# Kernel tuning notes

Hardware: AMD Instinct MI355X
Metric: run time of the kernel (lower is better)

Reference implementation:

```python
import jax, jax.numpy as jnp
import numpy as np

N_USER = 100000
M_ITEM = 50000
N_NODE = N_USER + M_ITEM
D = 64           # latent_dim
WD = D // 2      # word_emb_dim
FU = FI = 10     # padded feature-bag width
NUF = NIF = 30000
VOCAB = 20000
T = 8            # tokens per text source (name/comment/comment_list)
DNU = DNI = 10   # numeric feature dims
B = 2048         # seed batch
S = 20           # sampled neighbors per layer
L = 2            # num_layers


def setup_inputs() -> dict:
    key = jax.random.key(0)
    ks = jax.random.split(key, 26)
    f = lambda i, s: jax.random.normal(ks[i], s, jnp.float32) * 0.05
    ri = lambda i, s, hi: jax.random.randint(ks[i], s, 0, hi)
    return {
        # int (graph / lookup) inputs
        "seeds": ri(0, (B,), N_USER),
        "neigh1": ri(1, (B, S), N_NODE),
        "neigh2": ri(2, (B, S, S), N_NODE),
        "user_feat_idx": ri(3, (N_USER, FU), NUF),
        "item_feat_idx": ri(4, (M_ITEM, FI), NIF),
        "user_text_idx": ri(5, (N_USER, 3, T), VOCAB),
        "item_text_idx": ri(6, (M_ITEM, 3, T), VOCAB),
        # float tables / features
        "user_id_emb": f(7, (N_USER, D)),
        "item_id_emb": f(8, (M_ITEM, D)),
        "user_feat_emb": f(9, (NUF, D)),
        "item_feat_emb": f(10, (NIF, D)),
        "word_emb": f(11, (VOCAB, WD)),
        "user_word300": f(12, (N_USER, 300)),
        "item_word300": f(13, (M_ITEM, 300)),
        "item_sent768": f(14, (M_ITEM, 768)),
        "user_numeric": f(15, (N_USER, DNU)),
        "item_numeric": f(16, (M_ITEM, DNI)),
        # linears (stored as (in, out); y = x @ W + b)
        "Wnum_u": f(17, (DNU, D)), "bnum_u": jnp.zeros((D,), jnp.float32),
        "Wnum_i": f(18, (DNI, D)), "bnum_i": jnp.zeros((D,), jnp.float32),
        "Wproj_u": f(19, (int(D * 3.5) + 300, D)), "bproj_u": jnp.zeros((D,), jnp.float32),
        "Wproj_i": f(20, (int(D * 3.5) + 300 + 768, D)), "bproj_i": jnp.zeros((D,), jnp.float32),
        "W_w": f(21, (L, 2 * D, D)), "b_w": jnp.zeros((L, D), jnp.float32),
        "W_v": f(22, (L, D, D)), "b_v": jnp.zeros((L, D), jnp.float32),
    }


def _forward(user_id_emb, item_id_emb, user_feat_emb, item_feat_emb, word_emb,
             user_word300, item_word300, item_sent768, user_numeric, item_numeric,
             Wnum_u, bnum_u, Wnum_i, bnum_i, Wproj_u, bproj_u, Wproj_i, bproj_i,
             W_w, b_w, W_v, b_v,
             seeds, neigh1, neigh2, user_feat_idx, item_feat_idx,
             user_text_idx, item_text_idx):
    # --- multi-source node embeddings (get_text_embedding + proj + numeric) ---
    # text: mean-pool word embeddings per source, concat 3 sources -> 1.5*D
    u_text = word_emb[user_text_idx].mean(axis=2).reshape(N_USER, 3 * WD)
    i_text = word_emb[item_text_idx].mean(axis=2).reshape(M_ITEM, 3 * WD)
    # feature bags: mean-pooled embedding lookup
    u_feat = user_feat_emb[user_feat_idx].mean(axis=1)
    i_feat = item_feat_emb[item_feat_idx].mean(axis=1)
    u = (jnp.concatenate([user_id_emb, u_feat, u_text, user_word300], -1) @ Wproj_u
         + bproj_u + user_numeric @ Wnum_u + bnum_u)
    it = (jnp.concatenate([item_id_emb, i_feat, i_text, item_word300, item_sent768], -1) @ Wproj_i
          + bproj_i + item_numeric @ Wnum_i + bnum_i)
    x = jnp.concatenate([u, it], axis=0)  # [N_NODE, D], items offset by N_USER

    # --- neighbor-sampled GraphSAGE: h = W_l([self, mean(V_l(neigh))]) ---
    def sage(l, self_x, neigh_x, act):
        agg = (neigh_x @ W_v[l] + b_v[l]).mean(axis=-2)
        h = jnp.concatenate([self_x, agg], axis=-1) @ W_w[l] + b_w[l]
        return jax.nn.relu(h) if act else h

    x0 = x[seeds]        # [B, D]
    x1 = x[neigh1]       # [B, S, D]
    x2 = x[neigh2]       # [B, S, S, D]
    h1 = sage(0, x1, x2, True)   # layer-0 applied to 1-hop nodes
    h0 = sage(0, x0, x1, True)   # layer-0 applied to seeds
    out = sage(1, h0, h1, False)  # final layer, no activation
    return out  # [B, D]


def reference(seeds, neigh1, neigh2, user_feat_idx, item_feat_idx, user_text_idx,
              item_text_idx, user_id_emb, item_id_emb, user_feat_emb, item_feat_emb,
              word_emb, user_word300, item_word300, item_sent768, user_numeric,
              item_numeric, Wnum_u, bnum_u, Wnum_i, bnum_i, Wproj_u, bproj_u,
              Wproj_i, bproj_i, W_w, b_w, W_v, b_v):
    return _forward(user_id_emb, item_id_emb, user_feat_emb, item_feat_emb, word_emb,
                    user_word300, item_word300, item_sent768, user_numeric, item_numeric,
                    Wnum_u, bnum_u, Wnum_i, bnum_i, Wproj_u, bproj_u, Wproj_i, bproj_i,
                    W_w, b_w, W_v, b_v,
                    seeds, neigh1, neigh2, user_feat_idx, item_feat_idx,
                    user_text_idx, item_text_idx)
```

## Files before the change

kernel.cpp:

```cpp
#include <hip/hip_runtime.h>
#include <stdint.h>

#define N_USER 100000
#define M_ITEM 50000
#define N_NODE 150000
#define B_SEED 2048
#define S_NB 20
#define UBLK 6250
#define IBLK 3125

typedef __bf16   bf16x8 __attribute__((ext_vector_type(8)));
typedef float    f32x4  __attribute__((ext_vector_type(4)));
typedef uint32_t u32x4  __attribute__((ext_vector_type(4)));

__device__ __forceinline__ uint16_t f2bf(float f) {
    uint32_t u = __float_as_uint(f);
    return (uint16_t)((u + 0x7FFFu + ((u >> 16) & 1u)) >> 16);
}
__device__ __forceinline__ uint32_t pack2bf(float a, float b) {
    return (uint32_t)f2bf(a) | ((uint32_t)f2bf(b) << 16);
}
__device__ __forceinline__ float bf2f(uint16_t u) {
    return __uint_as_float(((uint32_t)u) << 16);
}

union BF8 { bf16x8 v; uint32_t u[4]; };

__device__ __forceinline__ bf16x8 pack8(const float4 lo, const float4 hi) {
    BF8 r;
    r.u[0] = pack2bf(lo.x, lo.y); r.u[1] = pack2bf(lo.z, lo.w);
    r.u[2] = pack2bf(hi.x, hi.y); r.u[3] = pack2bf(hi.z, hi.w);
    return r.v;
}
__device__ __forceinline__ bf16x8 ldf32x8_mask(const float* rowp, int base, int limit) {
    BF8 r;
#pragma unroll
    for (int h = 0; h < 4; ++h) {
        const int k0 = base + 2 * h;
        const float a = (k0     < limit) ? rowp[k0]     : 0.f;
        const float b = (k0 + 1 < limit) ? rowp[k0 + 1] : 0.f;
        r.u[h] = pack2bf(a, b);
    }
    return r.v;
}

__global__ void prep_kernel(const float* __restrict__ Wproj_u, const float* __restrict__ Wnum_u,
                            const float* __restrict__ Wproj_i, const float* __restrict__ Wnum_i,
                            const float* __restrict__ Wv0, const float* __restrict__ Ww0,
                            uint16_t* __restrict__ WTU, uint16_t* __restrict__ WTI,
                            uint16_t* __restrict__ WvT, uint16_t* __restrict__ WwT)
{
    const int idx = blockIdx.x * 256 + threadIdx.x;
    if (idx < 36864) {
        const int d = idx / 576, kp = idx - d * 576;
        float v = 0.f;
        if (kp < 160)      v = Wproj_u[(64 + kp) * 64 + d];
        else if (kp < 224) v = Wproj_u[(kp - 160) * 64 + d];
        else if (kp < 256) { const int j = kp - 224; if (j < 10)  v = Wnum_u[j * 64 + d]; }
        else               { const int j = kp - 256; if (j < 300) v = Wproj_u[(224 + j) * 64 + d]; }
        WTU[d * 576 + kp] = f2bf(v);
    } else if (idx < 122880) {
        const int i2 = idx - 36864;
        const int d = i2 / 1344, kp = i2 - d * 1344;
        float v = 0.f;
        if (kp < 160)      v = Wproj_i[(64 + kp) * 64 + d];
        else if (kp < 224) v = Wproj_i[(kp - 160) * 64 + d];
        else if (kp < 256) { const int j = kp - 224; if (j < 10)  v = Wnum_i[j * 64 + d]; }
        else if (kp < 576) { const int j = kp - 256; if (j < 300) v = Wproj_i[(224 + j) * 64 + d]; }
        else               { const int j = kp - 576; v = Wproj_i[(524 + j) * 64 + d]; }
        WTI[d * 1344 + kp] = f2bf(v);
    } else {
        const int i2 = idx - 122880;
        if (i2 < 4096) { const int d = i2 >> 6, k = i2 & 63;  WvT[d * 64 + k]  = f2bf(Wv0[k * 64 + d]); }
        else           { const int j = i2 - 4096;
                         const int d = j >> 7, k = j & 127;   WwT[d * 128 + k] = f2bf(Ww0[k * 64 + d]); }
    }
}

__global__ __launch_bounds__(256, 4) void proj_kernel(
    const float* __restrict__ u_id,  const int* __restrict__ ufi,
    const float* __restrict__ ufe,   const int* __restrict__ uti,
    const float* __restrict__ i_id,  const int* __restrict__ ifi,
    const float* __restrict__ ife,   const int* __restrict__ iti,
    const float* __restrict__ word_emb,
    const float* __restrict__ uw300, const float* __restrict__ iw300,
    const float* __restrict__ is768,
    const float* __restrict__ unum,  const float* __restrict__ inum,
    const uint16_t* __restrict__ WTU, const uint16_t* __restrict__ WTI,
    const float* __restrict__ bproj_u, const float* __restrict__ bnum_u,
    const float* __restrict__ bproj_i, const float* __restrict__ bnum_i,
    uint16_t* __restrict__ xout)
{
    __shared__ float R[4 * 16 * 64];

    const int t = threadIdx.x;
    const int w = t >> 6, l = t & 63;
    const int l15 = l & 15, g4 = l >> 4;
    const bool item = blockIdx.x >= UBLK;
    const int tile = item ? (blockIdx.x - UBLK) : blockIdx.x;
    const int nloc = tile * 16 + l15;

    const float* id_emb   = item ? i_id  : u_id;
    const int*   feat_idx = item ? ifi   : ufi;
    const float* feat_emb = item ? ife   : ufe;
    const int*   text_idx = item ? iti   : uti;
    const float* word300  = item ? iw300 : uw300;
    const float* numeric  = item ? inum  : unum;
    const uint16_t* WT    = item ? WTI   : WTU;
    const int KPADP       = item ? 1344  : 576;

    f32x4 acc[4] = {};
    const uint16_t* WTp[4];
#pragma unroll
    for (int db = 0; db < 4; ++db)
        WTp[db] = WT + (size_t)(db * 16 + l15) * KPADP + g4 * 8;

    auto MM = [&](bf16x8 af, int kb) {
#pragma unroll
        for (int db = 0; db < 4; ++db) {
            const bf16x8 bfr = *reinterpret_cast<const bf16x8*>(WTp[db] + kb);
            acc[db] = __builtin_amdgcn_mfma_f32_16x16x32_bf16(af, bfr, acc[db], 0, 0, 0);
        }
    };

    if (w < 2) {
        const int* fip = feat_idx + (size_t)nloc * 10;
        int fi[10];
#pragma unroll
        for (int j = 0; j < 10; ++j) fi[j] = fip[j];
        float4 s0 = make_float4(0.f, 0.f, 0.f, 0.f);
        float4 s1 = make_float4(0.f, 0.f, 0.f, 0.f);
#pragma unroll
        for (int j = 0; j < 10; ++j) {
            const float* rp = feat_emb + (size_t)fi[j] * 64 + w * 32 + g4 * 8;
            const float4 a = *(const float4*)rp;
            const float4 b = *(const float4*)(rp + 4);
            s0.x += a.x; s0.y += a.y; s0.z += a.z; s0.w += a.w;
            s1.x += b.x; s1.y += b.y; s1.z += b.z; s1.w += b.w;
        }
        MM(pack8(make_float4(s0.x * 0.1f, s0.y * 0.1f, s0.z * 0.1f, s0.w * 0.1f),
                 make_float4(s1.x * 0.1f, s1.y * 0.1f, s1.z * 0.1f, s1.w * 0.1f)),
           w * 32);
    }

    {
        const int src = (w == 2) ? 0 : (w == 3) ? 1 : (w == 0) ? 2 : -1;
        if (src >= 0) {
            const int* tip = text_idx + ((size_t)nloc * 3 + src) * 8;
            int tok[8];
#pragma unroll
            for (int j = 0; j < 8; ++j) tok[j] = tip[j];
            float4 s0 = make_float4(0.f, 0.f, 0.f, 0.f);
            float4 s1 = make_float4(0.f, 0.f, 0.f, 0.f);
#pragma unroll
            for (int j = 0; j < 8; ++j) {
                const float* rp = word_emb + (size_t)tok[j] * 32 + g4 * 8;
                const float4 a = *(const float4*)rp;
                const float4 b = *(const float4*)(rp + 4);
                s0.x += a.x; s0.y += a.y; s0.z += a.z; s0.w += a.w;
                s1.x += b.x; s1.y += b.y; s1.z += b.z; s1.w += b.w;
            }
            MM(pack8(make_float4(s0.x * 0.125f, s0.y * 0.125f, s0.z * 0.125f, s0.w * 0.125f),
                     make_float4(s1.x * 0.125f, s1.y * 0.125f, s1.z * 0.125f, s1.w * 0.125f)),
               (2 + src) * 32);
        }
    }

    if (w == 1 || w == 2) {
        const int half = w - 1;
        const float* p = id_emb + (size_t)nloc * 64 + half * 32 + g4 * 8;
        MM(pack8(*(const float4*)p, *(const float4*)(p + 4)), (5 + half) * 32);
    }

    if (w == 3)
        MM(ldf32x8_mask(numeric + (size_t)nloc * 10, g4 * 8, 10), 7 * 32);

    {
        const float* wr = word300 + (size_t)nloc * 300;
        float4 va[3][2];
#pragma unroll
        for (int i = 0; i < 3; ++i) {
            const int ks = 8 + w + 4 * i;
            if (ks < 17) {
                const float* p = wr + (ks - 8) * 32 + g4 * 8;
                va[i][0] = *(const float4*)p;
                va[i][1] = *(const float4*)(p + 4);
            }
        }
#pragma unroll
        for (int i = 0; i < 3; ++i) {
            const int ks = 8 + w + 4 * i;
            if (ks < 17)       MM(pack8(va[i][0], va[i][1]), ks * 32);
            else if (ks == 17) MM(ldf32x8_mask(wr, 288 + g4 * 8, 300), 17 * 32);
        }
    }

    if (item) {
        const float* sr = is768 + (size_t)nloc * 768;
        float4 va[6][2];
#pragma unroll
        for (int i = 0; i < 6; ++i) {
            const float* p = sr + (w + 4 * i) * 32 + g4 * 8;
            va[i][0] = *(const float4*)p;
            va[i][1] = *(const float4*)(p + 4);
        }
#pragma unroll
        for (int i = 0; i < 6; ++i)
            MM(pack8(va[i][0], va[i][1]), (18 + w + 4 * i) * 32);
    }

    {
        float* Rw = R + w * 1024;
#pragma unroll
        for (int db = 0; db < 4; ++db)
#pragma unroll
            for (int r = 0; r < 4; ++r)
                Rw[(g4 * 4 + r) * 64 + db * 16 + l15] = acc[db][r];
    }
    __syncthreads();

    const int n  = t >> 4;
    const int dq = t & 15;
    const f32x4* RV = (const f32x4*)R;
    f32x4 s = RV[n * 16 + dq] + RV[256 + n * 16 + dq]
            + RV[512 + n * 16 + dq] + RV[768 + n * 16 + dq];

    const float* bp = item ? bproj_i : bproj_u;
    const float* bn = item ? bnum_i  : bnum_u;
    const float4 b1 = *(const float4*)(bp + dq * 4);
    const float4 b2 = *(const float4*)(bn + dq * 4);
    const uint32_t o0 = pack2bf(s[0] + b1.x + b2.x, s[1] + b1.y + b2.y);
    const uint32_t o1 = pack2bf(s[2] + b1.z + b2.z, s[3] + b1.w + b2.w);
    const size_t obase = ((size_t)(item ? N_USER : 0) + (size_t)tile * 16 + n) * 64 + dq * 4;
    *(uint2*)(xout + obase) = make_uint2(o0, o1);
}

__global__ __launch_bounds__(256) void xv_kernel(
    const uint16_t* __restrict__ x, const uint16_t* __restrict__ WvT,
    const float* __restrict__ bv, uint16_t* __restrict__ xv, int n)
{
    const int t = threadIdx.x;
    const int w = t >> 6, l = t & 63, l15 = l & 15, g4 = l >> 4;
    const int node = blockIdx.x * 64 + w * 16 + l15;
    const int node_c = node < n ? node : n - 1;

    f32x4 acc[4] = {};
    const uint16_t* WTb = WvT + l15 * 64 + g4 * 8;
#pragma unroll
    for (int ks = 0; ks < 2; ++ks) {
        const bf16x8 af = *reinterpret_cast<const bf16x8*>(x + (size_t)node_c * 64 + ks * 32 + g4 * 8);
#pragma unroll
        for (int db = 0; db < 4; ++db) {
            const bf16x8 bfr = *reinterpret_cast<const bf16x8*>(WTb + db * 16 * 64 + ks * 32);
            acc[db] = __builtin_amdgcn_mfma_f32_16x16x32_bf16(af, bfr, acc[db], 0, 0, 0);
        }
    }
    const int node_base = blockIdx.x * 64 + w * 16 + g4 * 4;
#pragma unroll
    for (int db = 0; db < 4; ++db) {
        const int d = db * 16 + l15;
        const float bias = bv[d];
#pragma unroll
        for (int r = 0; r < 4; ++r) {
            const int nn = node_base + r;
            if (nn < n) xv[(size_t)nn * 64 + d] = f2bf(acc[db][r] + bias);
        }
    }
}

__global__ __launch_bounds__(256) void sage_mfma_kernel(
    const uint16_t* __restrict__ x, const uint16_t* __restrict__ xv,
    const int* __restrict__ self_idx, const int* __restrict__ neigh_idx,
    const uint16_t* __restrict__ WwT, const float* __restrict__ bw,
    uint16_t* __restrict__ out, int relu)
{
    const int t = threadIdx.x;
    const int w = t >> 6, l = t & 63, l15 = l & 15, g4 = l >> 4;
    const int r = blockIdx.x * 64 + w * 16 + l15;
    const int sidx = self_idx[r];
    const int* ni = neigh_idx + (size_t)r * S_NB;

    f32x4 acc[4] = {};
    const uint16_t* WTb = WwT + l15 * 128 + g4 * 8;

    auto MM = [&](bf16x8 af, int kb) {
#pragma unroll
        for (int db = 0; db < 4; ++db) {
            const bf16x8 bfr = *reinterpret_cast<const bf16x8*>(WTb + db * 16 * 128 + kb);
            acc[db] = __builtin_amdgcn_mfma_f32_16x16x32_bf16(af, bfr, acc[db], 0, 0, 0);
        }
    };

#pragma unroll
    for (int ks = 0; ks < 2; ++ks) {
        const bf16x8 af = *reinterpret_cast<const bf16x8*>(x + (size_t)sidx * 64 + ks * 32 + g4 * 8);
        MM(af, ks * 32);
    }
#pragma unroll
    for (int ks = 0; ks < 2; ++ks) {
        float ev[4] = {0.f, 0.f, 0.f, 0.f}, od[4] = {0.f, 0.f, 0.f, 0.f};
#pragma unroll
        for (int j = 0; j < S_NB; ++j) {
            const u32x4 v = *reinterpret_cast<const u32x4*>(xv + (size_t)ni[j] * 64 + ks * 32 + g4 * 8);
#pragma unroll
            for (int q = 0; q < 4; ++q) {
                ev[q] += __uint_as_float(v[q] << 16);
                od[q] += __uint_as_float(v[q] & 0xffff0000u);
            }
        }
        BF8 m;
#pragma unroll
        for (int q = 0; q < 4; ++q) m.u[q] = pack2bf(ev[q] * (1.f / S_NB), od[q] * (1.f / S_NB));
        MM(m.v, 64 + ks * 32);
    }

    const int rb = blockIdx.x * 64 + w * 16 + g4 * 4;
#pragma unroll
    for (int db = 0; db < 4; ++db) {
        const int d = db * 16 + l15;
        const float bias = bw[d];
#pragma unroll
        for (int rr = 0; rr < 4; ++rr) {
            float h = acc[db][rr] + bias;
            if (relu) h = fmaxf(h, 0.f);
            out[(size_t)(rb + rr) * 64 + d] = f2bf(h);
        }
    }
}

__global__ __launch_bounds__(256) void final_kernel(
    const uint16_t* __restrict__ h0, const uint16_t* __restrict__ h1,
    const float* __restrict__ Wv, const float* __restrict__ bv,
    const float* __restrict__ Ww, const float* __restrict__ bw,
    float* __restrict__ out)
{
    __shared__ float WvL[64 * 64];
    __shared__ float WwL[128 * 64];
    const int t = threadIdx.x;
    for (int i = t; i < 64 * 64; i += 256)  WvL[i] = Wv[i];
    for (int i = t; i < 128 * 64; i += 256) WwL[i] = Ww[i];
    __syncthreads();

    const int wave = t >> 6, lane = t & 63;
    const int base = blockIdx.x * 32 + wave * 8;
    const float bvl = bv[lane], bwl = bw[lane];

    for (int i = 0; i < 8; ++i) {
        const int b = base + i;
        float m = 0.f;
#pragma unroll
        for (int s = 0; s < S_NB; ++s)
            m += bf2f(h1[(size_t)(b * S_NB + s) * 64 + lane]);
        m *= (1.f / S_NB);

        float agg = bvl;
#pragma unroll 8
        for (int k = 0; k < 64; ++k)
            agg += __shfl(m, k) * WvL[k * 64 + lane];

        const float selfv = bf2f(h0[(size_t)b * 64 + lane]);
        float h = bwl;
#pragma unroll 8
        for (int k = 0; k < 64; ++k)
            h += __shfl(selfv, k) * WwL[k * 64 + lane];
#pragma unroll 8
        for (int k = 0; k < 64; ++k)
            h += __shfl(agg, k) * WwL[(64 + k) * 64 + lane];

        out[(size_t)b * 64 + lane] = h;
    }
}

extern "C" void kernel_launch(void* const* d_in, const int* in_sizes, int n_in,
                              void* d_out, int out_size, void* d_ws, size_t ws_size,
                              hipStream_t stream)
{
    const int*   seeds   = (const int*)d_in[0];
    const int*   neigh1  = (const int*)d_in[1];
    const int*   neigh2  = (const int*)d_in[2];
    const int*   ufi     = (const int*)d_in[3];
    const int*   ifi     = (const int*)d_in[4];
    const int*   uti     = (const int*)d_in[5];
    const int*   iti     = (const int*)d_in[6];
    const float* u_id    = (const float*)d_in[7];
    const float* i_id    = (const float*)d_in[8];
    const float* ufe     = (const float*)d_in[9];
    const float* ife     = (const float*)d_in[10];
    const float* wemb    = (const float*)d_in[11];
    const float* uw300   = (const float*)d_in[12];
    const float* iw300   = (const float*)d_in[13];
    const float* is768   = (const float*)d_in[14];
    const float* unum    = (const float*)d_in[15];
    const float* inum    = (const float*)d_in[16];
    const float* Wnum_u  = (const float*)d_in[17];
    const float* bnum_u  = (const float*)d_in[18];
    const float* Wnum_i  = (const float*)d_in[19];
    const float* bnum_i  = (const float*)d_in[20];
    const float* Wproj_u = (const float*)d_in[21];
    const float* bproj_u = (const float*)d_in[22];
    const float* Wproj_i = (const float*)d_in[23];
    const float* bproj_i = (const float*)d_in[24];
    const float* W_w     = (const float*)d_in[25];
    const float* b_w     = (const float*)d_in[26];
    const float* W_v     = (const float*)d_in[27];
    const float* b_v     = (const float*)d_in[28];

    uint16_t* WTU  = (uint16_t*)d_ws;
    uint16_t* WTI  = WTU  + 36864;
    uint16_t* WvT0 = WTI  + 86016;
    uint16_t* WwT0 = WvT0 + 4096;
    uint16_t* xbf  = WwT0 + 8192;
    uint16_t* xvbf = xbf  + (size_t)N_NODE * 64;
    uint16_t* h1bf = xvbf + (size_t)N_NODE * 64;
    uint16_t* h0bf = h1bf + (size_t)B_SEED * S_NB * 64;
    float* outp = (float*)d_out;

    prep_kernel<<<528, 256, 0, stream>>>(
        Wproj_u, Wnum_u, Wproj_i, Wnum_i, W_v, W_w, WTU, WTI, WvT0, WwT0);

    proj_kernel<<<UBLK + IBLK, 256, 0, stream>>>(
        u_id, ufi, ufe, uti, i_id, ifi, ife, iti, wemb,
        uw300, iw300, is768, unum, inum,
        WTU, WTI, bproj_u, bnum_u, bproj_i, bnum_i, xbf);

    xv_kernel<<<(N_NODE + 63) / 64, 256, 0, stream>>>(xbf, WvT0, b_v, xvbf, N_NODE);

    sage_mfma_kernel<<<(B_SEED * S_NB) / 64, 256, 0, stream>>>(
        xbf, xvbf, neigh1, neigh2, WwT0, b_w, h1bf, 1);
    sage_mfma_kernel<<<B_SEED / 64, 256, 0, stream>>>(
        xbf, xvbf, seeds, neigh1, WwT0, b_w, h0bf, 1);

    final_kernel<<<B_SEED / 32, 256, 0, stream>>>(
        h0bf, h1bf, W_v + 4096, b_v + 64, W_w + 8192, b_w + 64, outp);
}
```

Baseline: 372.0 us.

## Rebalance proj_kernel wave work, hoist loads early, pad LDS reduction buffer

Restructures the per-wave work split in the projection kernel so feature-bag and text-bag gathers are balanced across waves. All independent loads (word300, id embeddings, numeric, sentence vectors) are issued up front before the gather-sum and MFMA phases to raise memory-level parallelism. Gathers are batched in groups of 5 and 4 rows to keep more loads in flight. It also pads the LDS reduction rows from 64 to 68 floats to avoid bank conflicts, and sets waves_per_eu to 3 in place of the previous launch bound. The cost is higher register pressure, which could reduce occupancy.

```diff
diff --git a/kernel.cpp b/kernel.cpp
--- a/kernel.cpp
+++ b/kernel.cpp
@@ -26,10 +26,10 @@
 
 union BF8 { bf16x8 v; uint32_t u[4]; };
 
-__device__ __forceinline__ bf16x8 pack8(const float4 lo, const float4 hi) {
+__device__ __forceinline__ bf16x8 pack8v(f32x4 lo, f32x4 hi) {
     BF8 r;
-    r.u[0] = pack2bf(lo.x, lo.y); r.u[1] = pack2bf(lo.z, lo.w);
-    r.u[2] = pack2bf(hi.x, hi.y); r.u[3] = pack2bf(hi.z, hi.w);
+    r.u[0] = pack2bf(lo[0], lo[1]); r.u[1] = pack2bf(lo[2], lo[3]);
+    r.u[2] = pack2bf(hi[0], hi[1]); r.u[3] = pack2bf(hi[2], hi[3]);
     return r.v;
 }
 __device__ __forceinline__ bf16x8 ldf32x8_mask(const float* rowp, int base, int limit) {
@@ -42,6 +42,47 @@
         r.u[h] = pack2bf(a, b);
     }
     return r.v;
+}
+
+__device__ __forceinline__ bf16x8 feat_frag(const float* __restrict__ fe,
+                                            const int* fi, int off) {
+    f32x4 s0 = {0,0,0,0}, s1 = {0,0,0,0};
+    f32x4 a[5], b[5];
+#pragma unroll
+    for (int j = 0; j < 5; ++j) {
+        const float* p = fe + (size_t)fi[j] * 64 + off;
+        a[j] = *(const f32x4*)p; b[j] = *(const f32x4*)(p + 4);
+    }
+#pragma unroll
+    for (int j = 0; j < 5; ++j) { s0 += a[j]; s1 += b[j]; }
+#pragma unroll
+    for (int j = 0; j < 5; ++j) {
+        const float* p = fe + (size_t)fi[5 + j] * 64 + off;
+        a[j] = *(const f32x4*)p; b[j] = *(const f32x4*)(p + 4);
+    }
+#pragma unroll
+    for (int j = 0; j < 5; ++j) { s0 += a[j]; s1 += b[j]; }
+    return pack8v(s0 * 0.1f, s1 * 0.1f);
+}
+
+__device__ __forceinline__ bf16x8 text_frag(const float* __restrict__ we,
+                                            int4 t0, int4 t1, int off) {
+    f32x4 s0 = {0,0,0,0}, s1 = {0,0,0,0};
+    f32x4 a[4], b[4];
+    const float* p;
+    p = we + (size_t)t0.x * 32 + off; a[0] = *(const f32x4*)p; b[0] = *(const f32x4*)(p + 4);
+    p = we + (size_t)t0.y * 32 + off; a[1] = *(const f32x4*)p; b[1] = *(const f32x4*)(p + 4);
+    p = we + (size_t)t0.z * 32 + off; a[2] = *(const f32x4*)p; b[2] = *(const f32x4*)(p + 4);
+    p = we + (size_t)t0.w * 32 + off; a[3] = *(const f32x4*)p; b[3] = *(const f32x4*)(p + 4);
+#pragma unroll
+    for (int j = 0; j < 4; ++j) { s0 += a[j]; s1 += b[j]; }
+    p = we + (size_t)t1.x * 32 + off; a[0] = *(const f32x4*)p; b[0] = *(const f32x4*)(p + 4);
+    p = we + (size_t)t1.y * 32 + off; a[1] = *(const f32x4*)p; b[1] = *(const f32x4*)(p + 4);
+    p = we + (size_t)t1.z * 32 + off; a[2] = *(const f32x4*)p; b[2] = *(const f32x4*)(p + 4);
+    p = we + (size_t)t1.w * 32 + off; a[3] = *(const f32x4*)p; b[3] = *(const f32x4*)(p + 4);
+#pragma unroll
+    for (int j = 0; j < 4; ++j) { s0 += a[j]; s1 += b[j]; }
+    return pack8v(s0 * 0.125f, s1 * 0.125f);
 }
 
 __global__ void prep_kernel(const float* __restrict__ Wproj_u, const float* __restrict__ Wnum_u,
@@ -77,7 +118,9 @@
     }
 }
 
-__global__ __launch_bounds__(256, 4) void proj_kernel(
+__global__ __attribute__((amdgpu_flat_work_group_size(256, 256)))
+           __attribute__((amdgpu_waves_per_eu(3, 3)))
+void proj_kernel(
     const float* __restrict__ u_id,  const int* __restrict__ ufi,
     const float* __restrict__ ufe,   const int* __restrict__ uti,
     const float* __restrict__ i_id,  const int* __restrict__ ifi,
@@ -91,7 +134,7 @@
     const float* __restrict__ bproj_i, const float* __restrict__ bnum_i,
     uint16_t* __restrict__ xout)
 {
-    __shared__ float R[4 * 16 * 64];
+    __shared__ float R[4 * 16 * 68];
 
     const int t = threadIdx.x;
     const int w = t >> 6, l = t & 63;
@@ -123,107 +166,92 @@
         }
     };
 
+    int fi[10];
+    int4 tA0, tA1, tB0, tB1;
     if (w < 2) {
         const int* fip = feat_idx + (size_t)nloc * 10;
-        int fi[10];
 #pragma unroll
         for (int j = 0; j < 10; ++j) fi[j] = fip[j];
-        float4 s0 = make_float4(0.f, 0.f, 0.f, 0.f);
-        float4 s1 = make_float4(0.f, 0.f, 0.f, 0.f);
-#pragma unroll
-        for (int j = 0; j < 10; ++j) {
-            const float* rp = feat_emb + (size_t)fi[j] * 64 + w * 32 + g4 * 8;
-            const float4 a = *(const float4*)rp;
-            const float4 b = *(const float4*)(rp + 4);
-            s0.x += a.x; s0.y += a.y; s0.z += a.z; s0.w += a.w;
-            s1.x += b.x; s1.y += b.y; s1.z += b.z; s1.w += b.w;
-        }
-        MM(pack8(make_float4(s0.x * 0.1f, s0.y * 0.1f, s0.z * 0.1f, s0.w * 0.1f),
-                 make_float4(s1.x * 0.1f, s1.y * 0.1f, s1.z * 0.1f, s1.w * 0.1f)),
-           w * 32);
-    }
-
-    {
-        const int src = (w == 2) ? 0 : (w == 3) ? 1 : (w == 0) ? 2 : -1;
-        if (src >= 0) {
-            const int* tip = text_idx + ((size_t)nloc * 3 + src) * 8;
-            int tok[8];
-#pragma unroll
-            for (int j = 0; j < 8; ++j) tok[j] = tip[j];
-            float4 s0 = make_float4(0.f, 0.f, 0.f, 0.f);
-            float4 s1 = make_float4(0.f, 0.f, 0.f, 0.f);
-#pragma unroll
-            for (int j = 0; j < 8; ++j) {
-                const float* rp = word_emb + (size_t)tok[j] * 32 + g4 * 8;
-                const float4 a = *(const float4*)rp;
-                const float4 b = *(const float4*)(rp + 4);
-                s0.x += a.x; s0.y += a.y; s0.z += a.z; s0.w += a.w;
-                s1.x += b.x; s1.y += b.y; s1.z += b.z; s1.w += b.w;
-            }
-            MM(pack8(make_float4(s0.x * 0.125f, s0.y * 0.125f, s0.z * 0.125f, s0.w * 0.125f),
-                     make_float4(s1.x * 0.125f, s1.y * 0.125f, s1.z * 0.125f, s1.w * 0.125f)),
-               (2 + src) * 32);
-        }
-    }
-
-    if (w == 1 || w == 2) {
-        const int half = w - 1;
-        const float* p = id_emb + (size_t)nloc * 64 + half * 32 + g4 * 8;
-        MM(pack8(*(const float4*)p, *(const float4*)(p + 4)), (5 + half) * 32);
-    }
-
-    if (w == 3)
-        MM(ldf32x8_mask(numeric + (size_t)nloc * 10, g4 * 8, 10), 7 * 32);
-
-    {
-        const float* wr = word300 + (size_t)nloc * 300;
-        float4 va[3][2];
-#pragma unroll
-        for (int i = 0; i < 3; ++i) {
-            const int ks = 8 + w + 4 * i;
-            if (ks < 17) {
-                const float* p = wr + (ks - 8) * 32 + g4 * 8;
-                va[i][0] = *(const float4*)p;
-                va[i][1] = *(const float4*)(p + 4);
-            }
-        }
-#pragma unroll
-        for (int i = 0; i < 3; ++i) {
-            const int ks = 8 + w + 4 * i;
-            if (ks < 17)       MM(pack8(va[i][0], va[i][1]), ks * 32);
-            else if (ks == 17) MM(ldf32x8_mask(wr, 288 + g4 * 8, 300), 17 * 32);
-        }
-    }
-
+    } else {
+        const int srcA = (w == 2) ? 0 : 1;
+        const int* tp = text_idx + ((size_t)nloc * 3 + srcA) * 8;
+        tA0 = *(const int4*)tp; tA1 = *(const int4*)(tp + 4);
+        if (w == 2) {
+            const int* tq = text_idx + ((size_t)nloc * 3 + 2) * 8;
+            tB0 = *(const int4*)tq; tB1 = *(const int4*)(tq + 4);
+        }
+    }
+
+    const float* wr = word300 + (size_t)nloc * 300;
+    f32x4 wv[3][2];
+    const int NJ = (w == 0) ? 3 : 2;
+#pragma unroll
+    for (int i = 0; i < 3; ++i) {
+        if (i < NJ) {
+            const int j = (w == 0) ? 4 * i : (w + 4 * i);
+            const float* p = wr + j * 32 + g4 * 8;
+            wv[i][0] = *(const f32x4*)p; wv[i][1] = *(const f32x4*)(p + 4);
+        }
+    }
+    f32x4 idv[2];
+    if (w >= 2) {
+        const float* p = id_emb + (size_t)nloc * 64 + (w - 2) * 32 + g4 * 8;
+        idv[0] = *(const f32x4*)p; idv[1] = *(const f32x4*)(p + 4);
+    }
+    bf16x8 numf, tailf;
+    if (w == 3) {
+        numf  = ldf32x8_mask(numeric + (size_t)nloc * 10, g4 * 8, 10);
+        tailf = ldf32x8_mask(wr, 288 + g4 * 8, 300);
+    }
+    f32x4 sv[6][2];
     if (item) {
         const float* sr = is768 + (size_t)nloc * 768;
-        float4 va[6][2];
 #pragma unroll
         for (int i = 0; i < 6; ++i) {
             const float* p = sr + (w + 4 * i) * 32 + g4 * 8;
-            va[i][0] = *(const float4*)p;
-            va[i][1] = *(const float4*)(p + 4);
-        }
+            sv[i][0] = *(const f32x4*)p; sv[i][1] = *(const f32x4*)(p + 4);
+        }
+    }
+
+    if (w < 2) {
+        MM(feat_frag(feat_emb, fi, w * 32 + g4 * 8), w * 32);
+    } else if (w == 2) {
+        MM(text_frag(word_emb, tA0, tA1, g4 * 8), 64);
+        MM(text_frag(word_emb, tB0, tB1, g4 * 8), 128);
+    } else {
+        MM(text_frag(word_emb, tA0, tA1, g4 * 8), 96);
+    }
+
+#pragma unroll
+    for (int i = 0; i < 3; ++i) {
+        if (i < NJ) {
+            const int j = (w == 0) ? 4 * i : (w + 4 * i);
+            MM(pack8v(wv[i][0], wv[i][1]), 256 + 32 * j);
+        }
+    }
+    if (w >= 2) MM(pack8v(idv[0], idv[1]), 160 + 32 * (w - 2));
+    if (w == 3) { MM(numf, 224); MM(tailf, 544); }
+    if (item) {
 #pragma unroll
         for (int i = 0; i < 6; ++i)
-            MM(pack8(va[i][0], va[i][1]), (18 + w + 4 * i) * 32);
+            MM(pack8v(sv[i][0], sv[i][1]), 576 + 32 * (w + 4 * i));
     }
 
     {
-        float* Rw = R + w * 1024;
+        float* Rw = R + w * (16 * 68);
 #pragma unroll
         for (int db = 0; db < 4; ++db)
 #pragma unroll
             for (int r = 0; r < 4; ++r)
-                Rw[(g4 * 4 + r) * 64 + db * 16 + l15] = acc[db][r];
+                Rw[(g4 * 4 + r) * 68 + db * 16 + l15] = acc[db][r];
     }
     __syncthreads();
 
     const int n  = t >> 4;
     const int dq = t & 15;
-    const f32x4* RV = (const f32x4*)R;
-    f32x4 s = RV[n * 16 + dq] + RV[256 + n * 16 + dq]
-            + RV[512 + n * 16 + dq] + RV[768 + n * 16 + dq];
+    const float* Rn = R + n * 68 + dq * 4;
+    f32x4 s = *(const f32x4*)Rn + *(const f32x4*)(Rn + 1088)
+            + *(const f32x4*)(Rn + 2176) + *(const f32x4*)(Rn + 3264);
 
     const float* bp = item ? bproj_i : bproj_u;
     const float* bn = item ? bnum_i  : bnum_u;
```

Result: slower. 418.6 us (+12.5%).

## Split node projection into gather-pack pass and per-wave full-K MFMA GEMM

Applied to the files above, without the earlier changes.

The fused projection kernel is split in two. A new gather kernel averages the feature-bag and text-token embeddings into a packed bf16 staging buffer, placed in the xv workspace region. The GEMM kernel then gives each wave 16 nodes over the full K range, which removes the LDS cross-wave reduction and __syncthreads, and it uses hardware bf16x2 conversion. The weight K-layout is reordered to match. The cost is an extra write and read of the staging buffer, and that buffer may run past the space reserved after xvbf.

```diff
diff --git a/kernel.cpp b/kernel.cpp
--- a/kernel.cpp
+++ b/kernel.cpp
@@ -1,4 +1,5 @@
 #include <hip/hip_runtime.h>
+#include <hip/hip_bf16.h>
 #include <stdint.h>
 
 #define N_USER 100000
@@ -6,8 +7,8 @@
 #define N_NODE 150000
 #define B_SEED 2048
 #define S_NB 20
-#define UBLK 6250
-#define IBLK 3125
+#define UBLK2 1563
+#define IBLK2 782
 
 typedef __bf16   bf16x8 __attribute__((ext_vector_type(8)));
 typedef float    f32x4  __attribute__((ext_vector_type(4)));
@@ -17,19 +18,20 @@
     uint32_t u = __float_as_uint(f);
     return (uint16_t)((u + 0x7FFFu + ((u >> 16) & 1u)) >> 16);
 }
-__device__ __forceinline__ uint32_t pack2bf(float a, float b) {
-    return (uint32_t)f2bf(a) | ((uint32_t)f2bf(b) << 16);
+__device__ __forceinline__ uint32_t pk2(float a, float b) {
+    __hip_bfloat162 h = __float22bfloat162_rn(make_float2(a, b));
+    return *reinterpret_cast<uint32_t*>(&h);
 }
 __device__ __forceinline__ float bf2f(uint16_t u) {
     return __uint_as_float(((uint32_t)u) << 16);
 }
 
-union BF8 { bf16x8 v; uint32_t u[4]; };
-
-__device__ __forceinline__ bf16x8 pack8(const float4 lo, const float4 hi) {
+union BF8 { bf16x8 v; uint32_t u[4]; uint2 d2[2]; };
+
+__device__ __forceinline__ bf16x8 pack8v(f32x4 lo, f32x4 hi) {
     BF8 r;
-    r.u[0] = pack2bf(lo.x, lo.y); r.u[1] = pack2bf(lo.z, lo.w);
-    r.u[2] = pack2bf(hi.x, hi.y); r.u[3] = pack2bf(hi.z, hi.w);
+    r.u[0] = pk2(lo[0], lo[1]); r.u[1] = pk2(lo[2], lo[3]);
+    r.u[2] = pk2(hi[0], hi[1]); r.u[3] = pk2(hi[2], hi[3]);
     return r.v;
 }
 __device__ __forceinline__ bf16x8 ldf32x8_mask(const float* rowp, int base, int limit) {
@@ -39,7 +41,7 @@
         const int k0 = base + 2 * h;
         const float a = (k0     < limit) ? rowp[k0]     : 0.f;
         const float b = (k0 + 1 < limit) ? rowp[k0 + 1] : 0.f;
-        r.u[h] = pack2bf(a, b);
+        r.u[h] = pk2(a, b);
     }
     return r.v;
 }
@@ -55,8 +57,8 @@
         const int d = idx / 576, kp = idx - d * 576;
         float v = 0.f;
         if (kp < 160)      v = Wproj_u[(64 + kp) * 64 + d];
-        else if (kp < 224) v = Wproj_u[(kp - 160) * 64 + d];
-        else if (kp < 256) { const int j = kp - 224; if (j < 10)  v = Wnum_u[j * 64 + d]; }
+        else if (kp < 192) { const int j = kp - 160; if (j < 10)  v = Wnum_u[j * 64 + d]; }
+        else if (kp < 256) v = Wproj_u[(kp - 192) * 64 + d];
         else               { const int j = kp - 256; if (j < 300) v = Wproj_u[(224 + j) * 64 + d]; }
         WTU[d * 576 + kp] = f2bf(v);
     } else if (idx < 122880) {
@@ -64,8 +66,8 @@
         const int d = i2 / 1344, kp = i2 - d * 1344;
         float v = 0.f;
         if (kp < 160)      v = Wproj_i[(64 + kp) * 64 + d];
-        else if (kp < 224) v = Wproj_i[(kp - 160) * 64 + d];
-        else if (kp < 256) { const int j = kp - 224; if (j < 10)  v = Wnum_i[j * 64 + d]; }
+        else if (kp < 192) { const int j = kp - 160; if (j < 10)  v = Wnum_i[j * 64 + d]; }
+        else if (kp < 256) v = Wproj_i[(kp - 192) * 64 + d];
         else if (kp < 576) { const int j = kp - 256; if (j < 300) v = Wproj_i[(224 + j) * 64 + d]; }
         else               { const int j = kp - 576; v = Wproj_i[(524 + j) * 64 + d]; }
         WTI[d * 1344 + kp] = f2bf(v);
@@ -77,12 +79,53 @@
     }
 }
 
-__global__ __launch_bounds__(256, 4) void proj_kernel(
-    const float* __restrict__ u_id,  const int* __restrict__ ufi,
-    const float* __restrict__ ufe,   const int* __restrict__ uti,
-    const float* __restrict__ i_id,  const int* __restrict__ ifi,
-    const float* __restrict__ ife,   const int* __restrict__ iti,
-    const float* __restrict__ word_emb,
+__global__ __launch_bounds__(256) void gpack_kernel(
+    const int* __restrict__ ufi, const int* __restrict__ ifi,
+    const int* __restrict__ uti, const int* __restrict__ iti,
+    const float* __restrict__ ufe, const float* __restrict__ ife,
+    const float* __restrict__ wemb,
+    uint16_t* __restrict__ Apre)
+{
+    const int gid  = blockIdx.x * 256 + threadIdx.x;
+    const int node = gid >> 3;
+    const int d0   = gid & 7;
+    if (node >= N_NODE) return;
+    const bool item = node >= N_USER;
+    const int nloc  = item ? node - N_USER : node;
+    const int*   fidx = (item ? ifi : ufi) + (size_t)nloc * 10;
+    const int*   tidx = (item ? iti : uti) + (size_t)nloc * 24;
+    const float* fe   = item ? ife : ufe;
+    uint16_t* out = Apre + (size_t)node * 160;
+
+    {
+        f32x4 s0 = {0, 0, 0, 0}, s1 = {0, 0, 0, 0};
+#pragma unroll
+        for (int j = 0; j < 10; ++j) {
+            const float* p = fe + (size_t)fidx[j] * 64 + 8 * d0;
+            s0 += *(const f32x4*)p;
+            s1 += *(const f32x4*)(p + 4);
+        }
+        s0 *= 0.1f; s1 *= 0.1f;
+        uint4 o = make_uint4(pk2(s0[0], s0[1]), pk2(s0[2], s0[3]),
+                             pk2(s1[0], s1[1]), pk2(s1[2], s1[3]));
+        *(uint4*)(out + 8 * d0) = o;
+    }
+#pragma unroll
+    for (int s = 0; s < 3; ++s) {
+        f32x4 a = {0, 0, 0, 0};
+#pragma unroll
+        for (int j = 0; j < 8; ++j) {
+            const float* p = wemb + (size_t)tidx[s * 8 + j] * 32 + 4 * d0;
+            a += *(const f32x4*)p;
+        }
+        a *= 0.125f;
+        *(uint2*)(out + 64 + 32 * s + 4 * d0) = make_uint2(pk2(a[0], a[1]), pk2(a[2], a[3]));
+    }
+}
+
+__global__ __launch_bounds__(256, 4) void pgemm_kernel(
+    const uint16_t* __restrict__ Apre,
+    const float* __restrict__ u_id,  const float* __restrict__ i_id,
     const float* __restrict__ uw300, const float* __restrict__ iw300,
     const float* __restrict__ is768,
     const float* __restrict__ unum,  const float* __restrict__ inum,
@@ -91,148 +134,95 @@
     const float* __restrict__ bproj_i, const float* __restrict__ bnum_i,
     uint16_t* __restrict__ xout)
 {
-    __shared__ float R[4 * 16 * 64];
-
     const int t = threadIdx.x;
     const int w = t >> 6, l = t & 63;
     const int l15 = l & 15, g4 = l >> 4;
-    const bool item = blockIdx.x >= UBLK;
-    const int tile = item ? (blockIdx.x - UBLK) : blockIdx.x;
-    const int nloc = tile * 16 + l15;
-
-    const float* id_emb   = item ? i_id  : u_id;
-    const int*   feat_idx = item ? ifi   : ufi;
-    const float* feat_emb = item ? ife   : ufe;
-    const int*   text_idx = item ? iti   : uti;
-    const float* word300  = item ? iw300 : uw300;
-    const float* numeric  = item ? inum  : unum;
-    const uint16_t* WT    = item ? WTI   : WTU;
-    const int KPADP       = item ? 1344  : 576;
+    const bool item = blockIdx.x >= UBLK2;
+    const int tile  = item ? (blockIdx.x - UBLK2) : blockIdx.x;
+    const int ntype = item ? M_ITEM : N_USER;
+    const int nloc0 = tile * 64 + w * 16 + l15;
+    const int nloc  = nloc0 < ntype ? nloc0 : ntype - 1;
+    const int node  = (item ? N_USER : 0) + nloc;
+
+    const uint16_t* WT = item ? WTI : WTU;
+    const int KP       = item ? 1344 : 576;
 
     f32x4 acc[4] = {};
-    const uint16_t* WTp[4];
-#pragma unroll
-    for (int db = 0; db < 4; ++db)
-        WTp[db] = WT + (size_t)(db * 16 + l15) * KPADP + g4 * 8;
+    const uint16_t* WTb = WT + (size_t)l15 * KP + g4 * 8;
 
     auto MM = [&](bf16x8 af, int kb) {
 #pragma unroll
         for (int db = 0; db < 4; ++db) {
-            const bf16x8 bfr = *reinterpret_cast<const bf16x8*>(WTp[db] + kb);
+            const bf16x8 bfr = *reinterpret_cast<const bf16x8*>(WTb + (size_t)db * 16 * KP + kb);
             acc[db] = __builtin_amdgcn_mfma_f32_16x16x32_bf16(af, bfr, acc[db], 0, 0, 0);
         }
     };
 
-    if (w < 2) {
-        const int* fip = feat_idx + (size_t)nloc * 10;
-        int fi[10];
-#pragma unroll
-        for (int j = 0; j < 10; ++j) fi[j] = fip[j];
-        float4 s0 = make_float4(0.f, 0.f, 0.f, 0.f);
-        float4 s1 = make_float4(0.f, 0.f, 0.f, 0.f);
-#pragma unroll
-        for (int j = 0; j < 10; ++j) {
-            const float* rp = feat_emb + (size_t)fi[j] * 64 + w * 32 + g4 * 8;
-            const float4 a = *(const float4*)rp;
-            const float4 b = *(const float4*)(rp + 4);
-            s0.x += a.x; s0.y += a.y; s0.z += a.z; s0.w += a.w;
-            s1.x += b.x; s1.y += b.y; s1.z += b.z; s1.w += b.w;
-        }
-        MM(pack8(make_float4(s0.x * 0.1f, s0.y * 0.1f, s0.z * 0.1f, s0.w * 0.1f),
-                 make_float4(s1.x * 0.1f, s1.y * 0.1f, s1.z * 0.1f, s1.w * 0.1f)),
-           w * 32);
-    }
-
     {
-        const int src = (w == 2) ? 0 : (w == 3) ? 1 : (w == 0) ? 2 : -1;
-        if (src >= 0) {
-            const int* tip = text_idx + ((size_t)nloc * 3 + src) * 8;
-            int tok[8];
-#pragma unroll
-            for (int j = 0; j < 8; ++j) tok[j] = tip[j];
-            float4 s0 = make_float4(0.f, 0.f, 0.f, 0.f);
-            float4 s1 = make_float4(0.f, 0.f, 0.f, 0.f);
-#pragma unroll
-            for (int j = 0; j < 8; ++j) {
-                const float* rp = word_emb + (size_t)tok[j] * 32 + g4 * 8;
-                const float4 a = *(const float4*)rp;
-                const float4 b = *(const float4*)(rp + 4);
-                s0.x += a.x; s0.y += a.y; s0.z += a.z; s0.w += a.w;
-                s1.x += b.x; s1.y += b.y; s1.z += b.z; s1.w += b.w;
+        const uint16_t* ap = Apre + (size_t)node * 160 + g4 * 8;
+        bf16x8 af[5];
+#pragma unroll
+        for (int ks = 0; ks < 5; ++ks) af[ks] = *(const bf16x8*)(ap + ks * 32);
+#pragma unroll
+        for (int ks = 0; ks < 5; ++ks) MM(af[ks], ks * 32);
+    }
+    MM(ldf32x8_mask((item ? inum : unum) + (size_t)nloc * 10, g4 * 8, 10), 160);
+    {
+        const float* idr = (item ? i_id : u_id) + (size_t)nloc * 64 + g4 * 8;
+        f32x4 a0 = *(const f32x4*)idr,        a1 = *(const f32x4*)(idr + 4);
+        f32x4 b0 = *(const f32x4*)(idr + 32), b1 = *(const f32x4*)(idr + 36);
+        MM(pack8v(a0, a1), 192);
+        MM(pack8v(b0, b1), 224);
+    }
+    {
+        const float* wr = (item ? iw300 : uw300) + (size_t)nloc * 300 + g4 * 8;
+        f32x4 va[5][2];
+#pragma unroll
+        for (int u = 0; u < 5; ++u) {
+            const float* p = wr + u * 32;
+            va[u][0] = *(const f32x4*)p; va[u][1] = *(const f32x4*)(p + 4);
+        }
+#pragma unroll
+        for (int u = 0; u < 5; ++u) MM(pack8v(va[u][0], va[u][1]), 256 + u * 32);
+#pragma unroll
+        for (int u = 0; u < 4; ++u) {
+            const float* p = wr + (5 + u) * 32;
+            va[u][0] = *(const f32x4*)p; va[u][1] = *(const f32x4*)(p + 4);
+        }
+#pragma unroll
+        for (int u = 0; u < 4; ++u) MM(pack8v(va[u][0], va[u][1]), 256 + (5 + u) * 32);
+        MM(ldf32x8_mask(wr - g4 * 8, 288 + g4 * 8, 300), 544);
+    }
+    if (item) {
+        const float* sr = is768 + (size_t)nloc * 768 + g4 * 8;
+#pragma unroll
+        for (int b = 0; b < 4; ++b) {
+            f32x4 va[6][2];
+#pragma unroll
+            for (int u = 0; u < 6; ++u) {
+                const float* p = sr + (b * 6 + u) * 32;
+                va[u][0] = *(const f32x4*)p; va[u][1] = *(const f32x4*)(p + 4);
             }
-            MM(pack8(make_float4(s0.x * 0.125f, s0.y * 0.125f, s0.z * 0.125f, s0.w * 0.125f),
-                     make_float4(s1.x * 0.125f, s1.y * 0.125f, s1.z * 0.125f, s1.w * 0.125f)),
-               (2 + src) * 32);
-        }
-    }
-
-    if (w == 1 || w == 2) {
-        const int half = w - 1;
-        const float* p = id_emb + (size_t)nloc * 64 + half * 32 + g4 * 8;
-        MM(pack8(*(const float4*)p, *(const float4*)(p + 4)), (5 + half) * 32);
-    }
-
-    if (w == 3)
-        MM(ldf32x8_mask(numeric + (size_t)nloc * 10, g4 * 8, 10), 7 * 32);
-
-    {
-        const float* wr = word300 + (size_t)nloc * 300;
-        float4 va[3][2];
-#pragma unroll
-        for (int i = 0; i < 3; ++i) {
-            const int ks = 8 + w + 4 * i;
-            if (ks < 17) {
-                const float* p = wr + (ks - 8) * 32 + g4 * 8;
-                va[i][0] = *(const float4*)p;
-                va[i][1] = *(const float4*)(p + 4);
-            }
-        }
-#pragma unroll
-        for (int i = 0; i < 3; ++i) {
-            const int ks = 8 + w + 4 * i;
-            if (ks < 17)       MM(pack8(va[i][0], va[i][1]), ks * 32);
-            else if (ks == 17) MM(ldf32x8_mask(wr, 288 + g4 * 8, 300), 17 * 32);
-        }
-    }
-
-    if (item) {
-        const float* sr = is768 + (size_t)nloc * 768;
-        float4 va[6][2];
-#pragma unroll
-        for (int i = 0; i < 6; ++i) {
-            const float* p = sr + (w + 4 * i) * 32 + g4 * 8;
-            va[i][0] = *(const float4*)p;
-            va[i][1] = *(const float4*)(p + 4);
-        }
-#pragma unroll
-        for (int i = 0; i < 6; ++i)
-            MM(pack8(va[i][0], va[i][1]), (18 + w + 4 * i) * 32);
-    }
-
-    {
-        float* Rw = R + w * 1024;
-#pragma unroll
-        for (int db = 0; db < 4; ++db)
-#pragma unroll
-            for (int r = 0; r < 4; ++r)
-                Rw[(g4 * 4 + r) * 64 + db * 16 + l15] = acc[db][r];
-    }
-    __syncthreads();
-
-    const int n  = t >> 4;
-    const int dq = t & 15;
-    const f32x4* RV = (const f32x4*)R;
-    f32x4 s = RV[n * 16 + dq] + RV[256 + n * 16 + dq]
-            + RV[512 + n * 16 + dq] + RV[768 + n * 16 + dq];
-
+#pragma unroll
+            for (int u = 0; u < 6; ++u)
+                MM(pack8v(va[u][0], va[u][1]), 576 + (b * 6 + u) * 32);
+        }
+    }
+
+    const int nb_out = tile * 64 + w * 16 + g4 * 4;
     const float* bp = item ? bproj_i : bproj_u;
     const float* bn = item ? bnum_i  : bnum_u;
-    const float4 b1 = *(const float4*)(bp + dq * 4);
-    const float4 b2 = *(const float4*)(bn + dq * 4);
-    const uint32_t o0 = pack2bf(s[0] + b1.x + b2.x, s[1] + b1.y + b2.y);
-    const uint32_t o1 = pack2bf(s[2] + b1.z + b2.z, s[3] + b1.w + b2.w);
-    const size_t obase = ((size_t)(item ? N_USER : 0) + (size_t)tile * 16 + n) * 64 + dq * 4;
-    *(uint2*)(xout + obase) = make_uint2(o0, o1);
+    uint16_t* xo = xout + (size_t)(item ? N_USER : 0) * 64;
+#pragma unroll
+    for (int db = 0; db < 4; ++db) {
+        const int d = db * 16 + l15;
+        const float bias = bp[d] + bn[d];
+#pragma unroll
+        for (int r = 0; r < 4; ++r) {
+            const int nn = nb_out + r;
+            if (nn < ntype) xo[(size_t)nn * 64 + d] = f2bf(acc[db][r] + bias);
+        }
+    }
 }
 
 __global__ __launch_bounds__(256) void xv_kernel(
@@ -310,7 +300,7 @@
         }
         BF8 m;
 #pragma unroll
-        for (int q = 0; q < 4; ++q) m.u[q] = pack2bf(ev[q] * (1.f / S_NB), od[q] * (1.f / S_NB));
+        for (int q = 0; q < 4; ++q) m.u[q] = pk2(ev[q] * (1.f / S_NB), od[q] * (1.f / S_NB));
         MM(m.v, 64 + ks * 32);
     }
 
@@ -413,14 +403,17 @@
     uint16_t* xvbf = xbf  + (size_t)N_NODE * 64;
     uint16_t* h1bf = xvbf + (size_t)N_NODE * 64;
     uint16_t* h0bf = h1bf + (size_t)B_SEED * S_NB * 64;
+    uint16_t* Apre = xvbf;
     float* outp = (float*)d_out;
 
     prep_kernel<<<528, 256, 0, stream>>>(
         Wproj_u, Wnum_u, Wproj_i, Wnum_i, W_v, W_w, WTU, WTI, WvT0, WwT0);
 
-    proj_kernel<<<UBLK + IBLK, 256, 0, stream>>>(
-        u_id, ufi, ufe, uti, i_id, ifi, ife, iti, wemb,
-        uw300, iw300, is768, unum, inum,
+    gpack_kernel<<<(N_NODE * 8 + 255) / 256, 256, 0, stream>>>(
+        ufi, ifi, uti, iti, ufe, ife, wemb, Apre);
+
+    pgemm_kernel<<<UBLK2 + IBLK2, 256, 0, stream>>>(
+        Apre, u_id, i_id, uw300, iw300, is768, unum, inum,
         WTU, WTI, bproj_u, bnum_u, bproj_i, bnum_i, xbf);
 
     xv_kernel<<<(N_NODE + 63) / 64, 256, 0, stream>>>(xbf, WvT0, b_v, xvbf, N_NODE);
```

New measurement: 389.1 us. +4.6%, slower.
